# Kernel tuning notes

Hardware: AMD Instinct MI355X
Metric: run time of the kernel (lower is better)

Reference implementation:

```python
import jax, jax.numpy as jnp
import numpy as np

N = 100000      # num nodes
DEG = 16        # uniform degree used to build the CSR indptr
E = N * DEG     # num edges
F_IN = 128
F_OUT = 32


def setup_inputs() -> dict:
    key = jax.random.key(0)
    k1, k2, k3, k4, k5 = jax.random.split(key, 5)
    X = jax.random.normal(k1, (N, F_IN), jnp.float32)
    # Linear layer params (torch nn.Linear default-ish scale)
    W = jax.random.normal(k2, (F_IN, F_OUT), jnp.float32) / np.sqrt(F_IN)
    b = jax.random.normal(k3, (F_OUT,), jnp.float32) * 0.01
    # CSR graph: uniform-degree indptr, random neighbors, normalized edge values
    row_pointers = jnp.arange(N + 1, dtype=jnp.int32) * DEG
    column_index = jax.random.randint(k4, (E,), 0, N, dtype=jnp.int32)
    degrees = jax.random.uniform(k5, (E,), jnp.float32)  # per-edge A_hat values
    return {"X": X, "W": W, "b": b, "row_pointers": row_pointers,
            "column_index": column_index, "degrees": degrees}


def reference(X, W, b, row_pointers, column_index, degrees):
    # X' = X W + b   (the nn.Linear)
    Xp = X @ W + b  # [N, F_OUT]
    num_edges = column_index.shape[0]
    # Recover row id of each CSR edge from indptr (generic, vectorized)
    row_ids = jnp.searchsorted(row_pointers,
                               jnp.arange(num_edges, dtype=row_pointers.dtype),
                               side='right') - 1  # [E]
    # SpMM: out[i] = sum_{e in row i} degrees[e] * Xp[column_index[e]]
    msgs = degrees[:, None] * Xp[column_index]  # [E, F_OUT]
    return jax.ops.segment_sum(msgs, row_ids, num_segments=row_pointers.shape[0] - 1)
```

## Files before the change

### kernel.cpp

```cpp
#include <hip/hip_runtime.h>

#define NN 100000
#define FIN 128
#define FOUT 32
#define DEG 16

typedef __bf16    bf16x8 __attribute__((ext_vector_type(8)));
typedef float     f32x4  __attribute__((ext_vector_type(4)));
typedef _Float16  h4     __attribute__((ext_vector_type(4)));

static __device__ __forceinline__ __bf16 f2bf(float f) {
    union { float f; unsigned u; } v; v.f = f;
    unsigned r = (v.u + 0x7FFFu + ((v.u >> 16) & 1u)) >> 16;
    union { unsigned short s; __bf16 b; } o; o.s = (unsigned short)r;
    return o.b;
}

__global__ __launch_bounds__(256) void gemm_xw(const float* __restrict__ X,
                                               const float* __restrict__ W,
                                               const float* __restrict__ bias,
                                               _Float16* __restrict__ Xp) {
    __shared__ __bf16 wt[FOUT][FIN + 8];
    const int tid = threadIdx.x;

#pragma unroll
    for (int q = 0; q < 4; ++q) {
        const int lin = (q * 256 + tid) * 4;
        const int k = lin >> 5;
        const int n = lin & 31;
        const float4 w4 = *reinterpret_cast<const float4*>(W + lin);
        wt[n + 0][k] = f2bf(w4.x);
        wt[n + 1][k] = f2bf(w4.y);
        wt[n + 2][k] = f2bf(w4.z);
        wt[n + 3][k] = f2bf(w4.w);
    }
    __syncthreads();

    const int wave   = blockIdx.x * (blockDim.x >> 6) + (tid >> 6);
    const int lane   = tid & 63;
    const int lane15 = lane & 15;
    const int quad   = lane >> 4;
    const int row0   = wave * 16;
    if (row0 >= NN) return;

    bf16x8 bfrag[2][4];
#pragma unroll
    for (int nt = 0; nt < 2; ++nt)
#pragma unroll
        for (int kb = 0; kb < 4; ++kb)
            bfrag[nt][kb] = *reinterpret_cast<const bf16x8*>(
                &wt[nt * 16 + lane15][kb * 32 + quad * 8]);

    const float bb0 = bias[lane15];
    const float bb1 = bias[16 + lane15];

    int m = row0 + lane15;
    if (m >= NN) m = NN - 1;
    const float* xrow = X + (size_t)m * FIN;

    f32x4 acc0 = {0.f, 0.f, 0.f, 0.f};
    f32x4 acc1 = {0.f, 0.f, 0.f, 0.f};

#pragma unroll
    for (int kb = 0; kb < 4; ++kb) {
        const float4 x0 = *reinterpret_cast<const float4*>(xrow + kb * 32 + quad * 8);
        const float4 x1 = *reinterpret_cast<const float4*>(xrow + kb * 32 + quad * 8 + 4);
        bf16x8 a;
        a[0] = f2bf(x0.x); a[1] = f2bf(x0.y); a[2] = f2bf(x0.z); a[3] = f2bf(x0.w);
        a[4] = f2bf(x1.x); a[5] = f2bf(x1.y); a[6] = f2bf(x1.z); a[7] = f2bf(x1.w);
        acc0 = __builtin_amdgcn_mfma_f32_16x16x32_bf16(a, bfrag[0][kb], acc0, 0, 0, 0);
        acc1 = __builtin_amdgcn_mfma_f32_16x16x32_bf16(a, bfrag[1][kb], acc1, 0, 0, 0);
    }

#pragma unroll
    for (int r = 0; r < 4; ++r) {
        const int row = row0 + quad * 4 + r;
        if (row < NN) {
            Xp[(size_t)row * FOUT + lane15]      = (_Float16)(acc0[r] + bb0);
            Xp[(size_t)row * FOUT + 16 + lane15] = (_Float16)(acc1[r] + bb1);
        }
    }
}

__global__ __launch_bounds__(256) void spmm_agg(const _Float16* __restrict__ Xp,
                                                const int* __restrict__ colidx,
                                                const float* __restrict__ deg,
                                                float* __restrict__ out) {
    const int t    = blockIdx.x * blockDim.x + threadIdx.x;
    const int node = t >> 3;
    const int f0   = (t & 7) * 4;
    if (node >= NN) return;

    const int e0 = node * DEG;

    const int4*   cp = reinterpret_cast<const int4*>(colidx + e0);
    const float4* dp = reinterpret_cast<const float4*>(deg + e0);
    int4   c4[4];
    float4 d4[4];
#pragma unroll
    for (int i = 0; i < 4; ++i) { c4[i] = cp[i]; d4[i] = dp[i]; }

    const int   cols[DEG] = { c4[0].x, c4[0].y, c4[0].z, c4[0].w,
                              c4[1].x, c4[1].y, c4[1].z, c4[1].w,
                              c4[2].x, c4[2].y, c4[2].z, c4[2].w,
                              c4[3].x, c4[3].y, c4[3].z, c4[3].w };
    const float ds[DEG]   = { d4[0].x, d4[0].y, d4[0].z, d4[0].w,
                              d4[1].x, d4[1].y, d4[1].z, d4[1].w,
                              d4[2].x, d4[2].y, d4[2].z, d4[2].w,
                              d4[3].x, d4[3].y, d4[3].z, d4[3].w };

    h4 v[DEG];
#pragma unroll
    for (int j = 0; j < DEG; ++j)
        v[j] = *reinterpret_cast<const h4*>(Xp + (size_t)cols[j] * FOUT + f0);

    float4 acc = {0.f, 0.f, 0.f, 0.f};
#pragma unroll
    for (int j = 0; j < DEG; ++j) {
        acc.x = fmaf(ds[j], (float)v[j][0], acc.x);
        acc.y = fmaf(ds[j], (float)v[j][1], acc.y);
        acc.z = fmaf(ds[j], (float)v[j][2], acc.z);
        acc.w = fmaf(ds[j], (float)v[j][3], acc.w);
    }
    *reinterpret_cast<float4*>(out + (size_t)node * FOUT + f0) = acc;
}

extern "C" void kernel_launch(void* const* d_in, const int* in_sizes, int n_in,
                              void* d_out, int out_size, void* d_ws, size_t ws_size,
                              hipStream_t stream) {
    const float* X      = (const float*)d_in[0];
    const float* W      = (const float*)d_in[1];
    const float* b      = (const float*)d_in[2];
    const int*   colidx = (const int*)d_in[4];
    const float* deg    = (const float*)d_in[5];
    float*       out    = (float*)d_out;
    _Float16*    Xp     = (_Float16*)d_ws;

    const int waves  = (NN + 15) / 16;
    const int blocks = (waves + 3) / 4;
    gemm_xw<<<blocks, 256, 0, stream>>>(X, W, b, Xp);

    const int blocks2 = (NN * 8 + 255) / 256;
    spmm_agg<<<blocks2, 256, 0, stream>>>(Xp, colidx, deg, out);
}
```

Measured before the change: 118.8 us.

## Split projected features into halves and pin each half to a group of XCDs

The GEMM now writes the projected features as two separate 16-column fp16 tables instead of one 32-column table. The SpMM remaps block indices so that blocks landing on XCDs 0-3 gather only from the first half and blocks on XCDs 4-7 only from the second. The aim is for each XCD's L2 to hold a smaller gather working set and so raise the hit rate of the random neighbor gathers. In exchange, the column-index and edge-weight arrays are read twice, once per half. The result also depends on blocks actually being dispatched round-robin across XCDs.

```diff
diff --git a/kernel.cpp b/kernel.cpp
--- a/kernel.cpp
+++ b/kernel.cpp
@@ -4,6 +4,7 @@
 #define FIN 128
 #define FOUT 32
 #define DEG 16
+#define HFEAT 16
 
 typedef __bf16    bf16x8 __attribute__((ext_vector_type(8)));
 typedef float     f32x4  __attribute__((ext_vector_type(4)));
@@ -19,7 +20,8 @@
 __global__ __launch_bounds__(256) void gemm_xw(const float* __restrict__ X,
                                                const float* __restrict__ W,
                                                const float* __restrict__ bias,
-                                               _Float16* __restrict__ Xp) {
+                                               _Float16* __restrict__ Xp0,
+                                               _Float16* __restrict__ Xp1) {
     __shared__ __bf16 wt[FOUT][FIN + 8];
     const int tid = threadIdx.x;
 
@@ -76,20 +78,27 @@
     for (int r = 0; r < 4; ++r) {
         const int row = row0 + quad * 4 + r;
         if (row < NN) {
-            Xp[(size_t)row * FOUT + lane15]      = (_Float16)(acc0[r] + bb0);
-            Xp[(size_t)row * FOUT + 16 + lane15] = (_Float16)(acc1[r] + bb1);
+            Xp0[(size_t)row * HFEAT + lane15] = (_Float16)(acc0[r] + bb0);
+            Xp1[(size_t)row * HFEAT + lane15] = (_Float16)(acc1[r] + bb1);
         }
     }
 }
 
-__global__ __launch_bounds__(256) void spmm_agg(const _Float16* __restrict__ Xp,
+__global__ __launch_bounds__(256) void spmm_agg(const _Float16* __restrict__ Xp0,
+                                                const _Float16* __restrict__ Xp1,
                                                 const int* __restrict__ colidx,
                                                 const float* __restrict__ deg,
                                                 float* __restrict__ out) {
-    const int t    = blockIdx.x * blockDim.x + threadIdx.x;
-    const int node = t >> 3;
-    const int f0   = (t & 7) * 4;
+    const int bi   = blockIdx.x;
+    const int xcd  = bi & 7;
+    const int half = xcd >> 2;
+    const int slot = (bi >> 3) * 4 + (xcd & 3);
+    const int lt   = threadIdx.x;
+    const int node = slot * 64 + (lt >> 2);
+    const int f0   = (lt & 3) * 4;
     if (node >= NN) return;
+
+    const _Float16* __restrict__ Xp = half ? Xp1 : Xp0;
 
     const int e0 = node * DEG;
 
@@ -112,7 +121,7 @@
     h4 v[DEG];
 #pragma unroll
     for (int j = 0; j < DEG; ++j)
-        v[j] = *reinterpret_cast<const h4*>(Xp + (size_t)cols[j] * FOUT + f0);
+        v[j] = *reinterpret_cast<const h4*>(Xp + (size_t)cols[j] * HFEAT + f0);
 
     float4 acc = {0.f, 0.f, 0.f, 0.f};
 #pragma unroll
@@ -122,7 +131,7 @@
         acc.z = fmaf(ds[j], (float)v[j][2], acc.z);
         acc.w = fmaf(ds[j], (float)v[j][3], acc.w);
     }
-    *reinterpret_cast<float4*>(out + (size_t)node * FOUT + f0) = acc;
+    *reinterpret_cast<float4*>(out + (size_t)node * FOUT + half * HFEAT + f0) = acc;
 }
 
 extern "C" void kernel_launch(void* const* d_in, const int* in_sizes, int n_in,
@@ -134,12 +143,13 @@
     const int*   colidx = (const int*)d_in[4];
     const float* deg    = (const float*)d_in[5];
     float*       out    = (float*)d_out;
-    _Float16*    Xp     = (_Float16*)d_ws;
+    _Float16*    Xp0    = (_Float16*)d_ws;
+    _Float16*    Xp1    = (_Float16*)d_ws + (size_t)NN * HFEAT;
 
     const int waves  = (NN + 15) / 16;
     const int blocks = (waves + 3) / 4;
-    gemm_xw<<<blocks, 256, 0, stream>>>(X, W, b, Xp);
+    gemm_xw<<<blocks, 256, 0, stream>>>(X, W, b, Xp0, Xp1);
 
-    const int blocks2 = (NN * 8 + 255) / 256;
-    spmm_agg<<<blocks2, 256, 0, stream>>>(Xp, colidx, deg, out);
+    const int blocks2 = 3128;
+    spmm_agg<<<blocks2, 256, 0, stream>>>(Xp0, Xp1, colidx, deg, out);
 }
```

Result: slower. 126.3 us (+6.2%).
